# Optimization experiments

Measured on AMD Instinct MI355X. Metric: run time of the kernel, lower is better.

The kernel has to match this reference:

```python
import jax, jax.numpy as jnp
import numpy as np

D = 1024      # in/out token dims
E = 2048      # expanded dim = 2*D
S_ATT = 128   # attention feature dim s
EPS = 1e-5
SQRT_S = np.sqrt(S_ATT).astype(np.float32)


def setup_inputs() -> dict:
    key = jax.random.key(0)
    ks = jax.random.split(key, 8)
    B, S = 4, 2048
    x = jax.random.normal(ks[0], (B, S, D), dtype=jnp.float32)
    pos_enc = jax.random.normal(ks[1], (S, S_ATT), dtype=jnp.float32)
    # uv Linear: xavier_uniform on weight of shape [2e+s, D]
    fan_out = 2 * E + S_ATT
    limit = np.sqrt(6.0 / (D + fan_out)).astype(np.float32)
    uv_w = jax.random.uniform(ks[2], (fan_out, D), dtype=jnp.float32, minval=-limit, maxval=limit)
    # o Linear: default kaiming-uniform-ish; plain uniform works for a reference
    lim_o = np.sqrt(1.0 / E).astype(np.float32)
    o_w = jax.random.uniform(ks[3], (D, E), dtype=jnp.float32, minval=-lim_o, maxval=lim_o)
    gamma = jax.random.uniform(ks[4], (2, S_ATT), dtype=jnp.float32)
    beta = jax.random.uniform(ks[5], (2, S_ATT), dtype=jnp.float32)
    ln_g = jnp.ones((), dtype=jnp.float32)          # ScaleNorm learnable scalar
    res_scale = jnp.ones((D,), dtype=jnp.float32)   # ChannelWiseScale
    return {"x": x, "pos_enc": pos_enc, "uv_w": uv_w, "o_w": o_w,
            "gamma": gamma, "beta": beta, "ln_g": ln_g, "res_scale": res_scale}


def _gau(x, pos_enc, uv_w, o_w, gamma, beta, ln_g, res_scale):
    # ScaleNorm: x / max(||x|| * d^-0.5, eps) * g
    norm = jnp.linalg.norm(x, axis=-1, keepdims=True) * (D ** -0.5)
    xn = x / jnp.maximum(norm, EPS) * ln_g
    uv = jax.nn.silu(jnp.einsum('bsd,fd->bsf', xn, uv_w))  # [B,S,2E+s]
    u, v, base = uv[..., :E], uv[..., E:2 * E], uv[..., 2 * E:]
    # per-head affine: base[...,None,:]*gamma+beta -> q,k
    qk_base = base[..., None, :] * gamma + beta             # [B,S,2,s]
    q = qk_base[..., 0, :] + pos_enc[None, :, :]            # 'add' pos enc
    k = qk_base[..., 1, :] + pos_enc[None, :, :]
    scores = jnp.einsum('bqs,bks->bqk', q, k) / SQRT_S
    kernel = jnp.square(jax.nn.relu(scores))                # squared-ReLU attention
    attn_v = jnp.einsum('bqk,bke->bqe', kernel, v)
    out = jnp.einsum('bqe,de->bqd', u * attn_v, o_w)
    # residual shortcut with channel-wise scale (in == out dims)
    return x * res_scale + out


def reference(x, pos_enc, uv_w, o_w, gamma, beta, ln_g, res_scale):
    return _gau(x, pos_enc, uv_w, o_w, gamma, beta, ln_g, res_scale)
```

## Files before the change

### kernel.cpp

```cpp
#include <hip/hip_runtime.h>

typedef unsigned short u16;
typedef __bf16 bf16x8 __attribute__((ext_vector_type(8)));
typedef float f32x4 __attribute__((ext_vector_type(4)));

#define SEQ   2048
#define DDIM  1024
#define EDIM  2048
#define FDIM  4224
#define SATT  128
#define NBATCH 4

__device__ __forceinline__ u16 f2bf(float f) {
  unsigned u = __float_as_uint(f);
  unsigned r = (u + 0x7fffu + ((u >> 16) & 1u)) >> 16;
  return (u16)r;
}
__device__ __forceinline__ float bf2f(u16 v) {
  return __uint_as_float(((unsigned)v) << 16);
}

__device__ __forceinline__ void gload16(const u16* g, u16* l) {
  auto gp = (const __attribute__((address_space(1))) u16*)(unsigned long long)g;
  auto lp = (__attribute__((address_space(3))) u16*)(unsigned)(unsigned long long)l;
  __builtin_amdgcn_global_load_lds(gp, lp, 16, 0, 0);
}


__global__ void cvt_bf16_kernel(const float* __restrict__ in, u16* __restrict__ out, int n4) {
  int i = blockIdx.x * blockDim.x + threadIdx.x;
  if (i >= n4) return;
  float4 v = reinterpret_cast<const float4*>(in)[i];
  unsigned p0 = (unsigned)f2bf(v.x) | ((unsigned)f2bf(v.y) << 16);
  unsigned p1 = (unsigned)f2bf(v.z) | ((unsigned)f2bf(v.w) << 16);
  uint2 pk; pk.x = p0; pk.y = p1;
  reinterpret_cast<uint2*>(out)[i] = pk;
}

__global__ void rms_kernel(const float* __restrict__ x, const float* __restrict__ ln_g,
                           u16* __restrict__ xn) {
  int row = blockIdx.x;
  int t = threadIdx.x;
  const float4* xr = reinterpret_cast<const float4*>(x + (size_t)row * DDIM);
  float4 v = xr[t];
  float s = v.x * v.x + v.y * v.y + v.z * v.z + v.w * v.w;
#pragma unroll
  for (int off = 32; off > 0; off >>= 1) s += __shfl_down(s, off);
  __shared__ float wsum[4];
  int lane = t & 63, wv = t >> 6;
  if (lane == 0) wsum[wv] = s;
  __syncthreads();
  float tot = wsum[0] + wsum[1] + wsum[2] + wsum[3];
  float rms = sqrtf(tot * (1.0f / (float)DDIM));
  float scale = ln_g[0] / fmaxf(rms, 1e-5f);
  unsigned p0 = (unsigned)f2bf(v.x * scale) | ((unsigned)f2bf(v.y * scale) << 16);
  unsigned p1 = (unsigned)f2bf(v.z * scale) | ((unsigned)f2bf(v.w * scale) << 16);
  uint2 pk; pk.x = p0; pk.y = p1;
  reinterpret_cast<uint2*>(xn + (size_t)row * DDIM)[t] = pk;
}

__global__ void qk_kernel(const u16* __restrict__ uv, const float* __restrict__ pos_enc,
                          const float* __restrict__ gamma, const float* __restrict__ beta,
                          u16* __restrict__ q, u16* __restrict__ k, int ldF) {
  int r = blockIdx.x;
  int t = threadIdx.x;
  int s = r & (SEQ - 1);
  float bval = bf2f(uv[(size_t)r * ldF + 2 * EDIM + t]);
  float pe = pos_enc[(size_t)s * SATT + t];
  float qv = bval * gamma[t] + beta[t] + pe;
  float kv = bval * gamma[SATT + t] + beta[SATT + t] + pe;
  q[(size_t)r * SATT + t] = f2bf(qv);
  k[(size_t)r * SATT + t] = f2bf(kv);
}

__global__ void transpose_v(const u16* __restrict__ uv, u16* __restrict__ vt, int ldF) {
  __shared__ u16 tile[32][33];
  int b = blockIdx.z;
  uv += (size_t)b * SEQ * ldF;
  vt += (size_t)b * EDIM * SEQ;
  int e0 = blockIdx.x * 32, s0 = blockIdx.y * 32;
  int tx = threadIdx.x, ty = threadIdx.y;
#pragma unroll
  for (int j = 0; j < 32; j += 8)
    tile[ty + j][tx] = uv[(size_t)(s0 + ty + j) * ldF + EDIM + e0 + tx];
  __syncthreads();
#pragma unroll
  for (int j = 0; j < 32; j += 8)
    vt[(size_t)(e0 + ty + j) * SEQ + s0 + tx] = tile[tx][ty + j];
}

template <int EPI>
__global__ __launch_bounds__(256, 2) void gemm_sm(
    const u16* __restrict__ A, const u16* __restrict__ B,
    int N, int K,
    u16* __restrict__ Cbf, float* __restrict__ Cf,
    const u16* __restrict__ U, int ldu,
    const float* __restrict__ Xres, const float* __restrict__ rscale,
    size_t sA, size_t sB, size_t sC, size_t sU) {
  __shared__ u16 lds[32768];
  const int tid = threadIdx.x;
  const int w = tid >> 6, l = tid & 63;
  const int wr = w >> 1, wc = w & 1;
  const int fr = l & 15, kg = l >> 4;

  const int bz = blockIdx.z;
  A += (size_t)bz * sA; B += (size_t)bz * sB; U += (size_t)bz * sU;

  const int nbx = gridDim.x;
  int li = blockIdx.y * nbx + blockIdx.x;
  const int cpx = (nbx * gridDim.y) >> 3;
  li = (li & 7) * cpx + (li >> 3);
  const int bn = li % nbx;
  const int bm = li / nbx;

  const int NT = K >> 6;

  const int cswz = (((l & 7) ^ (l >> 3)) & 7) << 3;
  const u16* pA = A + (size_t)bm * 128 * K + (size_t)((w << 3) + (l >> 3)) * K + cswz;
  const u16* pB = B + (size_t)bn * 128 * K + (size_t)((w << 3) + (l >> 3)) * K + cswz;

  const int X  = (l & 7) << 4;
  const int Y0 = (kg << 4) ^ X;
  const int Y1 = ((kg << 4) | 64) ^ X;
  const char* ldsC = (const char*)lds;
  const char* aR0 = ldsC + wr * 8192 + fr * 128 + Y0;
  const char* aR1 = ldsC + wr * 8192 + fr * 128 + Y1;
  const char* bR0 = ldsC + 16384 + wc * 8192 + fr * 128 + Y0;
  const char* bR1 = ldsC + 16384 + wc * 8192 + fr * 128 + Y1;

  auto stg = [&](int bufw, int isB, const u16* g, int ofs) {
    u16* base = lds + bufw * 16384 + isB * 8192 + w * 512;
#pragma unroll
    for (int L = 0; L < 4; L++)
      gload16(g + (size_t)(L * 32) * K + ofs, base + L * 2048);
  };

  f32x4 acc[4][4];
#pragma unroll
  for (int i = 0; i < 4; i++)
#pragma unroll
    for (int j = 0; j < 4; j++) acc[i][j] = f32x4{0.f, 0.f, 0.f, 0.f};

  stg(0, 0, pA, 0); stg(0, 1, pB, 0);
  asm volatile("s_waitcnt vmcnt(0)" ::: "memory");
  __builtin_amdgcn_s_barrier();
  __builtin_amdgcn_sched_barrier(0);

  bf16x8 aH[4][2], bF[4][2];

#define TILE_STEP(BUF, ST, OFS)                                               \
  {                                                                           \
    if (ST) { stg((BUF) ^ 1, 0, pA, OFS); stg((BUF) ^ 1, 1, pB, OFS); }       \
    _Pragma("unroll") for (int i = 0; i < 4; i++) {                           \
      aH[i][0] = *(const bf16x8*)(aR0 + (BUF) * 32768 + i * 2048);            \
      aH[i][1] = *(const bf16x8*)(aR1 + (BUF) * 32768 + i * 2048);            \
    }                                                                         \
    _Pragma("unroll") for (int j = 0; j < 4; j++) {                           \
      bF[j][0] = *(const bf16x8*)(bR0 + (BUF) * 32768 + j * 2048);            \
      bF[j][1] = *(const bf16x8*)(bR1 + (BUF) * 32768 + j * 2048);            \
    }                                                                         \
    _Pragma("unroll") for (int s = 0; s < 2; s++)                             \
    _Pragma("unroll") for (int i = 0; i < 4; i++)                             \
    _Pragma("unroll") for (int j = 0; j < 4; j++)                             \
      acc[i][j] = __builtin_amdgcn_mfma_f32_16x16x32_bf16(                    \
          aH[i][s], bF[j][s], acc[i][j], 0, 0, 0);                            \
    asm volatile("s_waitcnt vmcnt(0)" ::: "memory");                          \
    __builtin_amdgcn_s_barrier();                                             \
    __builtin_amdgcn_sched_barrier(0);                                        \
  }

  for (int t2 = 0; t2 < NT; t2 += 2) {
    const bool st0 = (t2 + 1 < NT);
    const bool st1 = (t2 + 2 < NT);
    TILE_STEP(0, st0, 64)
    TILE_STEP(1, st1, 128)
    pA += 128; pB += 128;
  }
#undef TILE_STEP

  const int m0 = bm * 128 + wr * 64;
  const int n0 = bn * 128 + wc * 64;
  const int rsub = (l >> 4) * 4;
  const int ccol = l & 15;
#pragma unroll
  for (int i = 0; i < 4; i++) {
#pragma unroll
    for (int j = 0; j < 4; j++) {
      int n = n0 + j * 16 + ccol;
#pragma unroll
      for (int tt = 0; tt < 4; tt++) {
        int m = m0 + i * 16 + rsub + tt;
        float v = acc[i][j][tt];
        size_t idx = (size_t)m * N + n;
        if constexpr (EPI == 0) {
          float sv = v / (1.f + __expf(-v));
          Cbf[(size_t)bz * sC + idx] = f2bf(sv);
        } else if constexpr (EPI == 1) {
          float sc = v * 0.08838834764831845f;
          sc = sc > 0.f ? sc * sc : 0.f;
          Cbf[(size_t)bz * sC + idx] = f2bf(sc);
        } else if constexpr (EPI == 2) {
          float uvl = bf2f(U[(size_t)m * ldu + n]);
          Cbf[(size_t)bz * sC + idx] = f2bf(v * uvl);
        } else {
          Cf[idx] = Xres[idx] * rscale[n] + v;
        }
      }
    }
  }
}

template <int EPI>
__global__ __launch_bounds__(256) void gemm_bt(
    const u16* __restrict__ A, const u16* __restrict__ B,
    int M, int N, int K,
    u16* __restrict__ Cbf, float* __restrict__ Cf,
    const u16* __restrict__ U, int ldu,
    const float* __restrict__ Xres, const float* __restrict__ rscale,
    size_t sA, size_t sB, size_t sC, size_t sU) {
  __shared__ u16 As[128 * 32];
  __shared__ u16 Bs[128 * 32];
  const int tid = threadIdx.x;
  const int wave = tid >> 6, lane = tid & 63;
  const int wr = wave >> 1, wc = wave & 1;
  const int bz = blockIdx.z;
  A += (size_t)bz * sA; B += (size_t)bz * sB; U += (size_t)bz * sU;
  const int nbx = gridDim.x;
  int li = blockIdx.y * nbx + blockIdx.x;
  const int cpx = (nbx * gridDim.y) >> 3;
  li = (li & 7) * cpx + (li >> 3);
  const int bn = li % nbx;
  const int bm = li / nbx;
  const size_t abase = (size_t)bm * 128 * K;
  const size_t bbase = (size_t)bn * 128 * K;
  const int srow = tid >> 2;
  const int scol = (tid & 3) * 8;
  f32x4 acc[4][4];
#pragma unroll
  for (int i = 0; i < 4; i++)
#pragma unroll
    for (int j = 0; j < 4; j++) acc[i][j] = f32x4{0.f, 0.f, 0.f, 0.f};
  const int fr = lane & 15;
  const int fk = (lane >> 4) * 8;
  for (int k0 = 0; k0 < K; k0 += 32) {
#pragma unroll
    for (int r = 0; r < 2; r++) {
      const u16* gA = A + abase + (size_t)(r * 64 + srow) * K + k0 + scol;
      const u16* gB = B + bbase + (size_t)(r * 64 + srow) * K + k0 + scol;
      gload16(gA, As + r * 2048 + wave * 512);
      gload16(gB, Bs + r * 2048 + wave * 512);
    }
    __syncthreads();
    bf16x8 af[4], bfr[4];
#pragma unroll
    for (int i = 0; i < 4; i++) {
      af[i]  = *reinterpret_cast<const bf16x8*>(&As[(wr * 64 + i * 16 + fr) * 32 + fk]);
      bfr[i] = *reinterpret_cast<const bf16x8*>(&Bs[(wc * 64 + i * 16 + fr) * 32 + fk]);
    }
#pragma unroll
    for (int i = 0; i < 4; i++)
#pragma unroll
      for (int j = 0; j < 4; j++)
        acc[i][j] = __builtin_amdgcn_mfma_f32_16x16x32_bf16(af[i], bfr[j], acc[i][j], 0, 0, 0);
    __syncthreads();
  }
  const int m0 = bm * 128 + wr * 64;
  const int n0 = bn * 128 + wc * 64;
  const int rsub = (lane >> 4) * 4;
  const int ccol = lane & 15;
#pragma unroll
  for (int i = 0; i < 4; i++) {
#pragma unroll
    for (int j = 0; j < 4; j++) {
      int n = n0 + j * 16 + ccol;
#pragma unroll
      for (int t = 0; t < 4; t++) {
        int m = m0 + i * 16 + rsub + t;
        float v = acc[i][j][t];
        size_t idx = (size_t)m * N + n;
        if constexpr (EPI == 0) {
          float sv = v / (1.f + __expf(-v));
          Cbf[(size_t)bz * sC + idx] = f2bf(sv);
        } else if constexpr (EPI == 1) {
          float sc = v * 0.08838834764831845f;
          sc = sc > 0.f ? sc * sc : 0.f;
          Cbf[(size_t)bz * sC + idx] = f2bf(sc);
        } else if constexpr (EPI == 2) {
          float uvl = bf2f(U[(size_t)m * ldu + n]);
          Cbf[(size_t)bz * sC + idx] = f2bf(v * uvl);
        } else {
          Cf[idx] = Xres[idx] * rscale[n] + v;
        }
      }
    }
  }
}


extern "C" void kernel_launch(void* const* d_in, const int* in_sizes, int n_in,
                              void* d_out, int out_size, void* d_ws, size_t ws_size,
                              hipStream_t stream) {
  const float* x        = (const float*)d_in[0];
  const float* pos_enc  = (const float*)d_in[1];
  const float* uv_w     = (const float*)d_in[2];
  const float* o_w      = (const float*)d_in[3];
  const float* gamma    = (const float*)d_in[4];
  const float* beta     = (const float*)d_in[5];
  const float* ln_g     = (const float*)d_in[6];
  const float* res_scale= (const float*)d_in[7];
  float* out = (float*)d_out;

  auto al = [](size_t b) { return (b + 255) & ~(size_t)255; };
  const size_t SZ_UVW  = (size_t)FDIM * DDIM * 2;
  const size_t SZ_OW   = (size_t)DDIM * EDIM * 2;
  const size_t SZ_Z    = (size_t)NBATCH * SEQ * EDIM * 2;
  const size_t SZ_XN   = (size_t)NBATCH * SEQ * DDIM * 2;
  const size_t SZ_UV   = (size_t)NBATCH * SEQ * FDIM * 2;
  const size_t SZ_QK   = (size_t)NBATCH * SEQ * SATT * 2;
  const size_t SZ_VT1  = (size_t)EDIM * SEQ * 2;
  const size_t SZ_P1   = (size_t)SEQ * SEQ * 2;
  const size_t need_full =
      al(SZ_UVW) + al(SZ_OW) + al(SZ_Z) + al(SZ_XN) + al(SZ_UV) + 2 * al(SZ_QK) +
      (size_t)NBATCH * (al(SZ_VT1) + al(SZ_P1));
  const bool FULL = ws_size >= need_full;

  char* p = (char*)d_ws;
  auto alloc = [&](size_t bytes) {
    char* r = p;
    p += (bytes + 255) & ~(size_t)255;
    return r;
  };

  if (FULL) {
    u16* uvw_bf = (u16*)alloc(SZ_UVW);
    u16* ow_bf  = (u16*)alloc(SZ_OW);
    u16* z      = (u16*)alloc(SZ_Z);
    u16* vt     = (u16*)alloc((size_t)NBATCH * al(SZ_VT1));
    u16* pmat   = (u16*)alloc((size_t)NBATCH * al(SZ_P1));
    u16* xn     = (u16*)alloc(SZ_XN);
    u16* uv     = (u16*)alloc(SZ_UV);
    u16* qb     = (u16*)alloc(SZ_QK);
    u16* kb     = (u16*)alloc(SZ_QK);
    const size_t sVT = al(SZ_VT1) >> 1;
    const size_t sP  = al(SZ_P1) >> 1;
    const int rows = NBATCH * SEQ;

    cvt_bf16_kernel<<<(FDIM * DDIM / 4 + 255) / 256, 256, 0, stream>>>(
        uv_w, uvw_bf, FDIM * DDIM / 4);
    cvt_bf16_kernel<<<(DDIM * EDIM / 4 + 255) / 256, 256, 0, stream>>>(
        o_w, ow_bf, DDIM * EDIM / 4);

    rms_kernel<<<rows, 256, 0, stream>>>(x, ln_g, xn);
    gemm_sm<0><<<dim3(FDIM / 128, rows / 128), 256, 0, stream>>>(
        xn, uvw_bf, FDIM, DDIM, uv, nullptr, nullptr, 0, nullptr, nullptr,
        0, 0, 0, 0);
    qk_kernel<<<rows, SATT, 0, stream>>>(uv, pos_enc, gamma, beta, qb, kb, FDIM);
    transpose_v<<<dim3(EDIM / 32, SEQ / 32, NBATCH), dim3(32, 8), 0, stream>>>(uv, vt, FDIM);
    gemm_sm<1><<<dim3(SEQ / 128, SEQ / 128, NBATCH), 256, 0, stream>>>(
        qb, kb, SEQ, SATT, pmat, nullptr, nullptr, 0, nullptr, nullptr,
        (size_t)SEQ * SATT, (size_t)SEQ * SATT, sP, 0);
    gemm_sm<2><<<dim3(EDIM / 128, SEQ / 128, NBATCH), 256, 0, stream>>>(
        pmat, vt, EDIM, SEQ, z, nullptr, uv, FDIM, nullptr, nullptr,
        sP, sVT, (size_t)SEQ * EDIM, (size_t)SEQ * FDIM);
    gemm_sm<3><<<dim3(DDIM / 128, rows / 128), 256, 0, stream>>>(
        z, ow_bf, DDIM, EDIM, nullptr, out, nullptr, 0, x, res_scale,
        0, 0, 0, 0);
    return;
  }

  u16* uvw_bf = (u16*)alloc(SZ_UVW);
  u16* ow_bf  = (u16*)alloc(SZ_OW);
  u16* z      = (u16*)alloc(SZ_Z);
  u16* vt     = (u16*)alloc(SZ_VT1);
  u16* pmat   = (u16*)alloc(SZ_P1);
  size_t fixed = (size_t)(p - (char*)d_ws);
  const size_t perbc = (size_t)SEQ * DDIM * 2 + (size_t)SEQ * FDIM * 2 +
                       2 * (size_t)SEQ * SATT * 2 + 4 * 256;
  int BC = (ws_size >= fixed + 4 * perbc) ? 4 : 1;
  u16* xn = (u16*)alloc((size_t)BC * SEQ * DDIM * 2);
  u16* uv = (u16*)alloc((size_t)BC * SEQ * FDIM * 2);
  u16* qb = (u16*)alloc((size_t)BC * SEQ * SATT * 2);
  u16* kb = (u16*)alloc((size_t)BC * SEQ * SATT * 2);

  cvt_bf16_kernel<<<(FDIM * DDIM / 4 + 255) / 256, 256, 0, stream>>>(
      uv_w, uvw_bf, FDIM * DDIM / 4);
  cvt_bf16_kernel<<<(DDIM * EDIM / 4 + 255) / 256, 256, 0, stream>>>(
      o_w, ow_bf, DDIM * EDIM / 4);

  for (int b0 = 0; b0 < NBATCH; b0 += BC) {
    int rows = BC * SEQ;
    rms_kernel<<<rows, 256, 0, stream>>>(x + (size_t)b0 * SEQ * DDIM, ln_g, xn);
    gemm_bt<0><<<dim3(FDIM / 128, rows / 128), 256, 0, stream>>>(
        xn, uvw_bf, rows, FDIM, DDIM, uv, nullptr, nullptr, 0, nullptr, nullptr,
        0, 0, 0, 0);
    qk_kernel<<<rows, SATT, 0, stream>>>(uv, pos_enc, gamma, beta, qb, kb, FDIM);
    for (int bb = 0; bb < BC; bb++) {
      int b = b0 + bb;
      const u16* uvb = uv + (size_t)bb * SEQ * FDIM;
      transpose_v<<<dim3(EDIM / 32, SEQ / 32, 1), dim3(32, 8), 0, stream>>>(uvb, vt, FDIM);
      gemm_bt<1><<<dim3(SEQ / 128, SEQ / 128), 256, 0, stream>>>(
          qb + (size_t)bb * SEQ * SATT, kb + (size_t)bb * SEQ * SATT,
          SEQ, SEQ, SATT, pmat, nullptr, nullptr, 0, nullptr, nullptr,
          0, 0, 0, 0);
      gemm_bt<2><<<dim3(EDIM / 128, SEQ / 128), 256, 0, stream>>>(
          pmat, vt, SEQ, EDIM, SEQ, z + (size_t)b * SEQ * EDIM, nullptr,
          uvb, FDIM, nullptr, nullptr, 0, 0, 0, 0);
    }
  }
  gemm_bt<3><<<dim3(DDIM / 128, (NBATCH * SEQ) / 128), 256, 0, stream>>>(
      z, ow_bf, NBATCH * SEQ, DDIM, EDIM, nullptr, out, nullptr, 0,
      x, res_scale, 0, 0, 0, 0);
}
```

Before: 274.7 us.

## Add 256x128 tiled GEMM kernel for uv, score and attn-V GEMMs

Introduces a new gemm_big kernel that computes 256x128 output tiles with each wave holding an 8x4 block of MFMA accumulators, double-buffered LDS staging with XOR swizzle, and grouped block reordering. It replaces the 128x128 gemm_sm for the uv projection, the QK score and the P·V GEMMs, aiming for more arithmetic per LDS and global load. The cost is higher register pressure (128 accumulator floats per thread), which may lower occupancy or cause spills. The kernel also gives up partial-tile handling: it relies on M being divisible by 256 and on the grid tile count being divisible by 8.

New measurement: 283.8 us. +3.3%, slower.

```diff
diff --git a/kernel.cpp b/kernel.cpp
--- a/kernel.cpp
+++ b/kernel.cpp
@@ -87,6 +87,117 @@
 #pragma unroll
   for (int j = 0; j < 32; j += 8)
     vt[(size_t)(e0 + ty + j) * SEQ + s0 + tx] = tile[tx][ty + j];
+}
+
+template <int EPI>
+__global__ __launch_bounds__(256, 2) void gemm_big(
+    const u16* __restrict__ A, const u16* __restrict__ B,
+    int N, int K,
+    u16* __restrict__ Cbf,
+    const u16* __restrict__ U, int ldu,
+    size_t sA, size_t sB, size_t sC, size_t sU) {
+  __shared__ u16 lds[2 * 12288];
+  const int tid = threadIdx.x;
+  const int w = tid >> 6, l = tid & 63;
+  const int wr = w >> 1, wc = w & 1;
+  const int fr = l & 15, kg = l >> 4;
+
+  const int bz = blockIdx.z;
+  A += (size_t)bz * sA; B += (size_t)bz * sB; U += (size_t)bz * sU;
+
+  const int nbx = gridDim.x;
+  int li = blockIdx.y * nbx + blockIdx.x;
+  const int cpx = (nbx * gridDim.y) >> 3;
+  li = (li & 7) * cpx + (li >> 3);
+  const int bn = li % nbx;
+  const int bm = li / nbx;
+
+  const int NT = K >> 5;
+
+  const int srow = (w << 4) + (l >> 2);
+  const int cswz = (((l & 3) ^ ((l >> 2) & 3)) << 3);
+  const u16* pA = A + (size_t)bm * 256 * K + (size_t)srow * K + cswz;
+  const u16* pB = B + (size_t)bn * 128 * K + (size_t)srow * K + cswz;
+
+  const int slot = ((kg ^ (fr & 3)) << 4);
+  const char* ldsC = (const char*)lds;
+  const char* aR = ldsC + wr * 8192 + fr * 64 + slot;
+  const char* bR = ldsC + 16384 + wc * 4096 + fr * 64 + slot;
+
+  auto stg = [&](int bufw, int ofs) {
+    u16* base = lds + bufw * 12288 + w * 512;
+#pragma unroll
+    for (int L = 0; L < 4; L++)
+      gload16(pA + (size_t)(L * 64) * K + ofs, base + L * 2048);
+#pragma unroll
+    for (int L = 0; L < 2; L++)
+      gload16(pB + (size_t)(L * 64) * K + ofs, base + 8192 + L * 2048);
+  };
+
+  f32x4 acc[8][4];
+#pragma unroll
+  for (int i = 0; i < 8; i++)
+#pragma unroll
+    for (int j = 0; j < 4; j++) acc[i][j] = f32x4{0.f, 0.f, 0.f, 0.f};
+
+  stg(0, 0);
+  asm volatile("s_waitcnt vmcnt(0)" ::: "memory");
+  __builtin_amdgcn_s_barrier();
+  __builtin_amdgcn_sched_barrier(0);
+
+  bf16x8 aH[8], bF[4];
+
+#define TILE_STEP(BUF, ST, OFS)                                               \
+  {                                                                           \
+    if (ST) stg((BUF) ^ 1, OFS);                                              \
+    _Pragma("unroll") for (int i = 0; i < 8; i++)                             \
+      aH[i] = *(const bf16x8*)(aR + (BUF) * 24576 + i * 1024);                \
+    _Pragma("unroll") for (int j = 0; j < 4; j++)                             \
+      bF[j] = *(const bf16x8*)(bR + (BUF) * 24576 + j * 1024);                \
+    _Pragma("unroll") for (int i = 0; i < 8; i++)                             \
+    _Pragma("unroll") for (int j = 0; j < 4; j++)                             \
+      acc[i][j] = __builtin_amdgcn_mfma_f32_16x16x32_bf16(                    \
+          aH[i], bF[j], acc[i][j], 0, 0, 0);                                  \
+    asm volatile("s_waitcnt vmcnt(0)" ::: "memory");                          \
+    __builtin_amdgcn_s_barrier();                                             \
+    __builtin_amdgcn_sched_barrier(0);                                        \
+  }
+
+  for (int t2 = 0; t2 < NT; t2 += 2) {
+    const bool st0 = (t2 + 1 < NT);
+    const bool st1 = (t2 + 2 < NT);
+    TILE_STEP(0, st0, 32)
+    TILE_STEP(1, st1, 64)
+    pA += 64; pB += 64;
+  }
+#undef TILE_STEP
+
+  const int rsub = (l >> 4) * 4;
+  const int ccol = l & 15;
+#pragma unroll
+  for (int i = 0; i < 8; i++) {
+#pragma unroll
+    for (int j = 0; j < 4; j++) {
+      int n = bn * 128 + wc * 64 + j * 16 + ccol;
+#pragma unroll
+      for (int tt = 0; tt < 4; tt++) {
+        int m = bm * 256 + wr * 128 + i * 16 + rsub + tt;
+        float v = acc[i][j][tt];
+        size_t idx = (size_t)m * N + n;
+        if constexpr (EPI == 0) {
+          float sv = v / (1.f + __expf(-v));
+          Cbf[(size_t)bz * sC + idx] = f2bf(sv);
+        } else if constexpr (EPI == 1) {
+          float sc = v * 0.08838834764831845f;
+          sc = sc > 0.f ? sc * sc : 0.f;
+          Cbf[(size_t)bz * sC + idx] = f2bf(sc);
+        } else {
+          float uvl = bf2f(U[(size_t)m * ldu + n]);
+          Cbf[(size_t)bz * sC + idx] = f2bf(v * uvl);
+        }
+      }
+    }
+  }
 }
 
 template <int EPI>
@@ -351,16 +462,15 @@
         o_w, ow_bf, DDIM * EDIM / 4);
 
     rms_kernel<<<rows, 256, 0, stream>>>(x, ln_g, xn);
-    gemm_sm<0><<<dim3(FDIM / 128, rows / 128), 256, 0, stream>>>(
-        xn, uvw_bf, FDIM, DDIM, uv, nullptr, nullptr, 0, nullptr, nullptr,
-        0, 0, 0, 0);
+    gemm_big<0><<<dim3(FDIM / 128, rows / 256), 256, 0, stream>>>(
+        xn, uvw_bf, FDIM, DDIM, uv, nullptr, 0, 0, 0, 0, 0);
     qk_kernel<<<rows, SATT, 0, stream>>>(uv, pos_enc, gamma, beta, qb, kb, FDIM);
     transpose_v<<<dim3(EDIM / 32, SEQ / 32, NBATCH), dim3(32, 8), 0, stream>>>(uv, vt, FDIM);
-    gemm_sm<1><<<dim3(SEQ / 128, SEQ / 128, NBATCH), 256, 0, stream>>>(
-        qb, kb, SEQ, SATT, pmat, nullptr, nullptr, 0, nullptr, nullptr,
+    gemm_big<1><<<dim3(SEQ / 128, SEQ / 256, NBATCH), 256, 0, stream>>>(
+        qb, kb, SEQ, SATT, pmat, nullptr, 0,
         (size_t)SEQ * SATT, (size_t)SEQ * SATT, sP, 0);
-    gemm_sm<2><<<dim3(EDIM / 128, SEQ / 128, NBATCH), 256, 0, stream>>>(
-        pmat, vt, EDIM, SEQ, z, nullptr, uv, FDIM, nullptr, nullptr,
+    gemm_big<2><<<dim3(EDIM / 128, SEQ / 256, NBATCH), 256, 0, stream>>>(
+        pmat, vt, EDIM, SEQ, z, uv, FDIM,
         sP, sVT, (size_t)SEQ * EDIM, (size_t)SEQ * FDIM);
     gemm_sm<3><<<dim3(DDIM / 128, rows / 128), 256, 0, stream>>>(
         z, ow_bf, DDIM, EDIM, nullptr, out, nullptr, 0, x, res_scale,
```
